# Optimization experiments

Measured on AMD Instinct MI355X. Metric: run time of the kernel, lower is better.

## Reference

```python
import jax, jax.numpy as jnp
import numpy as np
from jax import lax


def _l2n(t, eps=1e-12):
    n = jnp.sqrt(jnp.sum(t * t, axis=-1, keepdims=True))
    return t / jnp.maximum(n, eps)


def _ln(t, w, b, eps=1e-5):
    mu = jnp.mean(t, -1, keepdims=True)
    var = jnp.var(t, -1, keepdims=True)
    return (t - mu) / jnp.sqrt(var + eps) * w + b


def _unfold3(x):
    # nn.Unfold(kernel_size=3, padding=1, stride=1): [B,C,H,W] -> [B,C,9,H*W]
    B, C, H, W = x.shape
    xp = jnp.pad(x, ((0, 0), (0, 0), (1, 1), (1, 1)))
    pat = jnp.stack([xp[:, :, i:i + H, j:j + W] for i in range(3) for j in range(3)], axis=2)
    return pat.reshape(B, C, 9, H * W)


def _forward(x, norm1_w, norm1_b, q_w, q_b, kv_w, kv_b, temperature, query_embedding,
             learnable_tokens, learnable_bias, sr_w, sr_b, pln_w, pln_b, proj_w, proj_b,
             norm2_w, norm2_b, fc1_w, fc1_b, dw_w, dw_b, fc2_w, fc2_b):
    B, C, H, W = x.shape
    nh = temperature.shape[0]
    d = C // nh
    N = H * W
    K = 9  # local_len = window_size**2
    # norm1 (WithBias LayerNorm over channel dim, channels-last)
    y = _ln(x.reshape(B, C, N).transpose(0, 2, 1), norm1_w, norm1_b)  # [B,N,C]
    # ---- AggregatedAttention ----
    q = (y @ q_w.T + q_b).reshape(B, N, nh, d).transpose(0, 2, 1, 3)  # [B,h,N,d]
    qn = _l2n(q)
    qs = (qn + query_embedding) * jax.nn.softplus(temperature)
    kv = y @ kv_w.T + kv_b  # [B,N,2C]
    k_loc = _l2n(kv[..., :C].reshape(B, N, nh, d)).reshape(B, N, C)
    kvl = jnp.concatenate([k_loc, kv[..., C:]], -1).transpose(0, 2, 1).reshape(B, 2 * C, H, W)
    pat = _unfold3(kvl).reshape(B, 2 * nh, d, K, N).transpose(0, 1, 4, 2, 3)  # [B,2h,N,d,K]
    k_l, v_l = pat[:, :nh], pat[:, nh:]
    attn_local = jnp.einsum('bhnd,bhndk->bhnk', qs, k_l)  # [B,h,N,K]
    # pooled branch; sr_ratio=1 so adaptive_avg_pool2d is identity
    y4 = y.transpose(0, 2, 1).reshape(B, C, H, W)
    xp = jax.nn.gelu(jnp.einsum('oc,bchw->bohw', sr_w, y4) + sr_b[:, None, None], approximate=False)
    xp = _ln(xp.reshape(B, C, N).transpose(0, 2, 1), pln_w, pln_b)  # [B,pool_len,C]
    kvp = (xp @ kv_w.T + kv_b).reshape(B, N, 2 * nh, d).transpose(0, 2, 1, 3)
    k_p = _l2n(kvp[:, :nh])
    v_p = kvp[:, nh:]
    attn_pool = jnp.einsum('bhnd,bhmd->bhnm', qs, k_p)  # [B,h,N,pool_len]
    attn = jax.nn.softmax(jnp.concatenate([attn_local, attn_pool], -1), axis=-1)
    a_l, a_p = attn[..., :K], attn[..., K:]
    w_l = jnp.einsum('bhnd,hdk->bhnk', qn, learnable_tokens) + learnable_bias + a_l
    x_local = jnp.einsum('bhnk,bhndk->bhnd', w_l, v_l)
    x_pool = jnp.einsum('bhnm,bhmd->bhnd', a_p, v_p)
    xo = (x_local + x_pool).transpose(0, 2, 1, 3).reshape(B, N, C)
    # proj then raw torch-style reshape [B,N,C] -> [B,C,H,W] (memory reinterpretation)
    xo = (xo @ proj_w.T + proj_b).reshape(B, C, H, W)
    x = x + xo
    # ---- ConvolutionalGLU MLP ----
    hf = dw_b.shape[0]
    y2 = _ln(x.reshape(B, C, N).transpose(0, 2, 1), norm2_w, norm2_b).transpose(0, 2, 1).reshape(B, C, H, W)
    f1 = jnp.einsum('oc,bchw->bohw', fc1_w, y2) + fc1_b[:, None, None]
    a, v = f1[:, :hf], f1[:, hf:]
    dw = lax.conv_general_dilated(a, dw_w, (1, 1), ((1, 1), (1, 1)),
                                  feature_group_count=hf,
                                  dimension_numbers=('NCHW', 'OIHW', 'NCHW')) + dw_b[:, None, None]
    g = jax.nn.gelu(dw, approximate=False) * v
    out = jnp.einsum('oc,bchw->bohw', fc2_w, g) + fc2_b[:, None, None]
    return x + out


def setup_inputs() -> dict:
    key = jax.random.key(0)
    B, C, H, W = 2, 128, 56, 56
    nh, d, K = 4, 32, 9
    hf = int(2 * int(C * 4.0) / 3)  # 341
    ks = iter(jax.random.split(key, 16))
    rn = lambda shape, s=0.02: jax.random.normal(next(ks), shape, jnp.float32) * s
    return {
        'x': jax.random.normal(next(ks), (B, C, H, W), jnp.float32),
        'norm1_w': jnp.ones((C,), jnp.float32), 'norm1_b': jnp.zeros((C,), jnp.float32),
        'q_w': rn((C, C)), 'q_b': jnp.zeros((C,), jnp.float32),
        'kv_w': rn((2 * C, C)), 'kv_b': jnp.zeros((2 * C,), jnp.float32),
        'temperature': jnp.full((nh, 1, 1), float(np.log(np.exp(1.0 / 0.24) - 1.0)), jnp.float32),
        'query_embedding': rn((nh, 1, d)),
        'learnable_tokens': rn((nh, d, K)),
        'learnable_bias': jnp.zeros((nh, 1, K), jnp.float32),
        'sr_w': rn((C, C)), 'sr_b': jnp.zeros((C,), jnp.float32),
        'pln_w': jnp.ones((C,), jnp.float32), 'pln_b': jnp.zeros((C,), jnp.float32),
        'proj_w': rn((C, C)), 'proj_b': jnp.zeros((C,), jnp.float32),
        'norm2_w': jnp.ones((C,), jnp.float32), 'norm2_b': jnp.zeros((C,), jnp.float32),
        'fc1_w': rn((2 * hf, C)), 'fc1_b': jnp.zeros((2 * hf,), jnp.float32),
        'dw_w': rn((hf, 1, 3, 3)), 'dw_b': jnp.zeros((hf,), jnp.float32),
        'fc2_w': rn((C, hf)), 'fc2_b': jnp.zeros((C,), jnp.float32),
    }


def reference(x, norm1_w, norm1_b, q_w, q_b, kv_w, kv_b, temperature, query_embedding,
              learnable_tokens, learnable_bias, sr_w, sr_b, pln_w, pln_b, proj_w, proj_b,
              norm2_w, norm2_b, fc1_w, fc1_b, dw_w, dw_b, fc2_w, fc2_b):
    return _forward(x, norm1_w, norm1_b, q_w, q_b, kv_w, kv_b, temperature, query_embedding,
                    learnable_tokens, learnable_bias, sr_w, sr_b, pln_w, pln_b, proj_w, proj_b,
                    norm2_w, norm2_b, fc1_w, fc1_b, dw_w, dw_b, fc2_w, fc2_b)
```

## Files before the change

kernel.cpp:

```cpp
#include <hip/hip_runtime.h>
#include <hip/hip_bf16.h>

typedef __hip_bfloat16 bf16;
typedef short s8v __attribute__((ext_vector_type(8)));
typedef short s4v __attribute__((ext_vector_type(4)));
typedef float f4v __attribute__((ext_vector_type(4)));

#define DEVI __device__ __forceinline__

DEVI float cvt(float x){ return x; }
DEVI float cvt(bf16 x){ return __bfloat162float(x); }

DEVI void stg(float* p, float v){ *p = v; }
DEVI void stg(bf16* p, float v){ *p = __float2bfloat16(v); }

DEVI float gelu_exact(float x){
  return 0.5f*x*(1.0f + erff(x*0.70710678118654752440f));
}

constexpr int B_ = 2, C_ = 128, H_ = 56, W_ = 56, N_ = 3136, NH_ = 4, D_ = 32, HF_ = 341;
constexpr int ROWS_ = B_*N_;
constexpr int KF2 = 352;
constexpr int GQ_ = NH_*B_*N_;
constexpr int FW = 512;
constexpr int KSP = 8;
constexpr int SPLIT = 384;
constexpr int NTILE = 392;
constexpr float LOG2E = 1.4426950408889634f;
constexpr float E8L2  = 11.541560327111707f;

DEVI void ln_tile_body(int tile, int t, const float* __restrict__ x,
                       const float* __restrict__ w, const float* __restrict__ bia,
                       bf16* __restrict__ y, float* sm , float* st )
{
  int b = tile / 196, nb = (tile % 196) * 16;
  {
    int c = t >> 1, half = t & 1;
    const float* xp = x + ((long)b*C_ + c)*N_ + nb + half*8;
    f4v v0 = *(const f4v*)xp;
    f4v v1 = *(const f4v*)(xp + 4);
    #pragma unroll
    for (int j=0;j<4;j++){
      sm[c*17 + half*8 + j    ] = v0[j];
      sm[c*17 + half*8 + 4 + j] = v1[j];
    }
  }
  __syncthreads();
  {
    int i = t >> 4, k = t & 15;
    float s = 0.f, ss = 0.f;
    #pragma unroll
    for (int u=0;u<8;u++){
      float v = sm[(k + u*16)*17 + i];
      s += v; ss = fmaf(v,v,ss);
    }
    #pragma unroll
    for (int off=1; off<16; off<<=1){
      s  += __shfl_xor(s,  off);
      ss += __shfl_xor(ss, off);
    }
    if (k == 0){
      float mu  = s*(1.0f/128.0f);
      float var = fmaxf(ss*(1.0f/128.0f) - mu*mu, 0.f);
      st[i]      = mu;
      st[16 + i] = rsqrtf(var + 1e-5f);
    }
  }
  __syncthreads();
  {
    int i = t >> 4, c0 = (t & 15)*8;
    float mu = st[i], inv = st[16 + i];
    bf16 o8[8];
    #pragma unroll
    for (int j=0;j<8;j++){
      int c = c0 + j;
      o8[j] = __float2bfloat16((sm[c*17 + i] - mu)*inv*w[c] + bia[c]);
    }
    *(s8v*)(y + ((long)(b*N_ + nb + i))*C_ + c0) = *(const s8v*)o8;
  }
}

__global__ __launch_bounds__(256)
void ln_tile_kernel(const float* __restrict__ x, const float* __restrict__ w,
                    const float* __restrict__ bia, bf16* __restrict__ y)
{
  __shared__ float sm[128*17];
  __shared__ float st[32];
  ln_tile_body(blockIdx.x, threadIdx.x, x, w, bia, y, sm, st);
}

__global__ __launch_bounds__(256)
void head_kernel(const float* __restrict__ q_w, const float* __restrict__ kv_w,
                 const float* __restrict__ sr_w, const float* __restrict__ proj_w,
                 const float* __restrict__ fc1_w, const float* __restrict__ fc2_w,
                 const float* __restrict__ q_b, const float* __restrict__ kv_b,
                 const float* __restrict__ sr_b, const float* __restrict__ tokens,
                 bf16* __restrict__ out, float* __restrict__ bias_out,
                 float* __restrict__ tokt,
                 const float* __restrict__ x_in, const float* __restrict__ n1w,
                 const float* __restrict__ n1b, bf16* __restrict__ y)
{
  __shared__ float sm[128*17];
  __shared__ float st[32];
  if (blockIdx.x >= 216){
    ln_tile_body(blockIdx.x - 216, threadIdx.x, x_in, n1w, n1b, y, sm, st);
    return;
  }
  int t = blockIdx.x*256 + threadIdx.x;
  if (t < 42304){
    int t0 = t*4;
    const float* src;
    if      (t0 <  16384) src = q_w    + t0;
    else if (t0 <  49152) src = kv_w   + (t0-16384);
    else if (t0 <  65536) src = sr_w   + (t0-49152);
    else if (t0 <  81920) src = proj_w + (t0-65536);
    else                  src = fc1_w  + (t0-81920);
    f4v v = *(const f4v*)src;
    bf16 o4[4];
    #pragma unroll
    for (int j=0;j<4;j++) o4[j] = __float2bfloat16(v[j]);
    *(s4v*)(out + t0) = *(const s4v*)o4;
  } else if (t < 53568){
    int i = (t - 42304)*4;
    int m = i / KF2, kp = i % KF2;
    bf16 o4[4];
    #pragma unroll
    for (int j=0;j<4;j++)
      o4[j] = __float2bfloat16((kp+j < HF_) ? fc2_w[m*HF_ + kp + j] : 0.f);
    *(s4v*)(out + 169216 + i) = *(const s4v*)o4;
  } else if (t < 54080){
    int i = t - 53568;
    float bv = (i < 128) ? q_b[i] : (i < 384) ? kv_b[i-128] : sr_b[i-384];
    bias_out[i] = bv;
  } else if (t < 55232){
    int i = t - 54080;
    int hk = i >> 5, d = i & 31;
    int h = hk / 9, k = hk - h*9;
    tokt[i] = tokens[(h*D_ + d)*9 + k];
  }
}

template<int KT, int MODE, typename TC, int BM=64, int LDA=KT, int NCH=1>
__global__ __launch_bounds__(256)
void gemm_mfma(const bf16* __restrict__ A, const bf16* __restrict__ B,
               const float* __restrict__ bias, const float* __restrict__ res,
               TC* __restrict__ Cm, int M, int Nn,
               long sA, long sB, long sC, long sR,
               const float* __restrict__ qe, const float* __restrict__ temp,
               bf16* __restrict__ aux0, bf16* __restrict__ aux1)
{
  A  += (long)blockIdx.z * sA;
  B  += (long)blockIdx.z * sB;
  Cm += (long)blockIdx.z * sC;
  if (res) res += (long)blockIdx.z * sR;
  int lane = threadIdx.x & 63, w = threadIdx.x >> 6;
  int m = lane & 15, quad = lane >> 4;
  int n0 = blockIdx.x*64, m0 = blockIdx.y*BM;
  const bf16* ap[NCH];
  #pragma unroll
  for (int cc=0; cc<NCH; cc++){
    int ar = m0 + cc*64 + w*16 + m;
    if (ar >= M) ar = M-1;
    ap[cc] = A + (long)ar*LDA + quad*8;
  }
  const bf16* bp = B + (long)(n0 + m)*KT + quad*8;
  s8v a4[KT/32];
  if (MODE==7){
    float s=0.f, ssum=0.f;
    #pragma unroll
    for (int i=0;i<KT/32;i++){
      a4[i] = *(const s8v*)(ap[0] + i*32);
      #pragma unroll
      for (int j=0;j<8;j++){
        float v = cvt(((const bf16*)&a4[i])[j]);
        s += v; ssum = fmaf(v,v,ssum);
      }
    }
    s    += __shfl_xor(s,16);    s    += __shfl_xor(s,32);
    ssum += __shfl_xor(ssum,16); ssum += __shfl_xor(ssum,32);
    float mu  = s*(1.0f/128.0f);
    float var = fmaxf(ssum*(1.0f/128.0f) - mu*mu, 0.f);
    float inv = rsqrtf(var + 1e-5f);
    #pragma unroll
    for (int i=0;i<KT/32;i++){
      #pragma unroll
      for (int j=0;j<8;j++){
        int c = i*32 + quad*8 + j;
        float v = cvt(((const bf16*)&a4[i])[j]);
        ((bf16*)&a4[i])[j] = __float2bfloat16((v-mu)*inv*qe[c] + temp[c]);
      }
    }
  }
  f4v acc[NCH][4];
  #pragma unroll
  for (int cc=0; cc<NCH; cc++)
    #pragma unroll
    for (int s=0;s<4;s++) acc[cc][s] = (f4v){0.f,0.f,0.f,0.f};
  __builtin_amdgcn_s_setprio(1);
  #pragma unroll
  for (int k0 = 0; k0 < KT; k0 += 32){
    s8v bf[4];
    #pragma unroll
    for (int s=0;s<4;s++) bf[s] = *(const s8v*)(bp + (long)s*16*KT + k0);
    #pragma unroll
    for (int cc=0; cc<NCH; cc++){
      s8v af = (MODE==7) ? a4[k0/32] : *(const s8v*)(ap[cc] + k0);
      #pragma unroll
      for (int s=0;s<4;s++)
        acc[cc][s] = __builtin_amdgcn_mfma_f32_16x16x32_bf16(af, bf[s], acc[cc][s], 0, 0, 0);
    }
  }
  __builtin_amdgcn_s_setprio(0);
  if ((MODE==6 || MODE==7) && blockIdx.x < 2){
    int hA = blockIdx.x*2, hB = hA+1;
    float spA = 0.f, spB = 0.f;
    if (MODE==6){
      spA = log1pf(expf(temp[hA])) * LOG2E;
      spB = log1pf(expf(temp[hB])) * LOG2E;
    }
    #pragma unroll
    for (int cc=0; cc<NCH; cc++){
      #pragma unroll
      for (int r=0;r<4;r++){
        float v4[4];
        #pragma unroll
        for (int s=0;s<4;s++) v4[s] = acc[cc][s][r] + bias[n0 + s*16 + m];
        float ssA = v4[0]*v4[0] + v4[1]*v4[1];
        float ssB = v4[2]*v4[2] + v4[3]*v4[3];
        #pragma unroll
        for (int off=1; off<16; off<<=1){
          ssA += __shfl_xor(ssA, off);
          ssB += __shfl_xor(ssB, off);
        }
        float invA = 1.f/fmaxf(sqrtf(ssA), 1e-12f);
        float invB = 1.f/fmaxf(sqrtf(ssB), 1e-12f);
        int gm = m0 + cc*64 + w*16 + quad*4 + r;
        int b = gm / N_, n = gm % N_;
        #pragma unroll
        for (int s=0;s<4;s++){
          int h = (s<2) ? hA : hB;
          int d = (s&1)*16 + m;
          float v = v4[s] * ((s<2) ? invA : invB);
          if (MODE==6) v = (v + qe[h*D_ + d]) * ((s<2) ? spA : spB);
          aux0[((long)(b*NH_+h)*N_ + n)*D_ + d] = __float2bfloat16(v);
        }
      }
    }
    return;
  }
  if (MODE==6 && blockIdx.x >= 2 && blockIdx.x < 4){
    #pragma unroll
    for (int cc=0; cc<NCH; cc++){
      #pragma unroll
      for (int r=0;r<4;r++){
        float v4[4];
        #pragma unroll
        for (int s=0;s<4;s++) v4[s] = acc[cc][s][r] + bias[n0 + s*16 + m];
        float ssA = v4[0]*v4[0] + v4[1]*v4[1];
        float ssB = v4[2]*v4[2] + v4[3]*v4[3];
        #pragma unroll
        for (int off=1; off<16; off<<=1){
          ssA += __shfl_xor(ssA, off);
          ssB += __shfl_xor(ssB, off);
        }
        float invA = 1.f/fmaxf(sqrtf(ssA), 1e-12f);
        float invB = 1.f/fmaxf(sqrtf(ssB), 1e-12f);
        int gm = m0 + cc*64 + w*16 + quad*4 + r;
        #pragma unroll
        for (int s=0;s<4;s++){
          float v = v4[s] * ((s<2) ? invA : invB);
          stg(&Cm[(long)gm*Nn + n0 + s*16 + m], v);
        }
      }
    }
    return;
  }
  if (MODE==7){
    int gm0 = m0 + w*16 + quad*4;
    int b = gm0 / N_, nb = gm0 % N_;
    #pragma unroll
    for (int s=0;s<4;s++){
      int h = (blockIdx.x-2)*2 + (s>>1);
      int d = (s&1)*16 + m;
      bf16 p4[4];
      #pragma unroll
      for (int r=0;r<4;r++) p4[r] = __float2bfloat16(acc[0][s][r] + bias[n0 + s*16 + m]);
      *(s4v*)(aux1 + ((long)(b*NH_+h)*D_ + d)*N_ + nb) = *(const s4v*)p4;
    }
    return;
  }
  #pragma unroll
  for (int cc=0; cc<NCH; cc++){
    int m0c = m0 + cc*64;
    #pragma unroll
    for (int s=0;s<4;s++){
      int gn = n0 + s*16 + m;
      #pragma unroll
      for (int r=0;r<4;r++){
        int gm = m0c + w*16 + quad*4 + r;
        if (gm >= M) continue;
        float v = acc[cc][s][r];
        if (MODE==1 || MODE==4 || MODE==6) v += bias[gn];
        else                               v += bias[gm];
        if (MODE==6 && gn >= 384) v = gelu_exact(v);
        if (MODE==4 || MODE==5) v += res[(long)gm*Nn + gn];
        stg(&Cm[(long)gm*Nn + gn], v);
      }
    }
  }
}

__global__ __launch_bounds__(256)
void attn_part_kernel(const bf16* __restrict__ qs_, const bf16* __restrict__ kp_,
                      const bf16* __restrict__ vp_,
                      bf16* __restrict__ Op, float* __restrict__ Lp)
{
  int bh = blockIdx.y;
  int z  = blockIdx.z;
  int lane = threadIdx.x & 63;
  int w    = threadIdx.x >> 6;
  int m    = lane & 15, quad = lane >> 4;
  int base = blockIdx.x*256 + w*16;

  s8v af[4]; bool hasQ[4];
  #pragma unroll
  for (int ch=0; ch<4; ch++){
    int qq = base + ch*64;
    hasQ[ch] = (qq < N_);
    af[ch] = *(const s8v*)(qs_ + ((long)bh*N_ + (hasQ[ch] ? qq : base) + m)*D_ + quad*8);
  }
  const bf16* kpb = kp_ + (long)bh*N_*D_;
  const bf16* vpb = vp_ + (long)bh*D_*N_;
  int kperm = (m & 3) + 8*(m >> 2);
  const f4v CINIT = {-E8L2, -E8L2, -E8L2, -E8L2};
  f4v o0[4], o1[4];
  float l[4];
  #pragma unroll
  for (int ch=0; ch<4; ch++){
    o0[ch] = (f4v){0.f,0.f,0.f,0.f}; o1[ch] = (f4v){0.f,0.f,0.f,0.f};
    l[ch] = 0.f;
  }

  auto loadKV = [&](s8v* kf, s8v* vf, int t){
    kf[0] = *(const s8v*)(kpb + (long)(t + kperm     )*D_ + quad*8);
    kf[1] = *(const s8v*)(kpb + (long)(t + kperm +  4)*D_ + quad*8);
    kf[2] = *(const s8v*)(kpb + (long)(t + kperm + 32)*D_ + quad*8);
    kf[3] = *(const s8v*)(kpb + (long)(t + kperm + 36)*D_ + quad*8);
    vf[0] = *(const s8v*)(vpb + (long)(m     )*N_ + t      + quad*8);
    vf[1] = *(const s8v*)(vpb + (long)(16 + m)*N_ + t      + quad*8);
    vf[2] = *(const s8v*)(vpb + (long)(m     )*N_ + t + 32 + quad*8);
    vf[3] = *(const s8v*)(vpb + (long)(16 + m)*N_ + t + 32 + quad*8);
  };
  auto compute = [&](const s8v* kf, const s8v* vf){
    __builtin_amdgcn_s_setprio(1);
    #pragma unroll
    for (int ch=0; ch<4; ch++){
      f4v c[4];
      #pragma unroll
      for (int s=0;s<4;s++)
        c[s] = __builtin_amdgcn_mfma_f32_16x16x32_bf16(kf[s], af[ch], CINIT, 0, 0, 0);
      bf16 p8a[8], p8b[8];
      float ls = 0.f;
      #pragma unroll
      for (int r=0;r<4;r++){
        float ea = __builtin_amdgcn_exp2f(c[0][r]);
        float eb = __builtin_amdgcn_exp2f(c[1][r]);
        float ec = __builtin_amdgcn_exp2f(c[2][r]);
        float ed = __builtin_amdgcn_exp2f(c[3][r]);
        ls += (ea+eb) + (ec+ed);
        p8a[r] = __float2bfloat16(ea); p8a[4+r] = __float2bfloat16(eb);
        p8b[r] = __float2bfloat16(ec); p8b[4+r] = __float2bfloat16(ed);
      }
      l[ch] += ls;
      s8v pa = *(const s8v*)p8a, pb = *(const s8v*)p8b;
      o0[ch] = __builtin_amdgcn_mfma_f32_16x16x32_bf16(pa, vf[0], o0[ch], 0, 0, 0);
      o1[ch] = __builtin_amdgcn_mfma_f32_16x16x32_bf16(pa, vf[1], o1[ch], 0, 0, 0);
      o0[ch] = __builtin_amdgcn_mfma_f32_16x16x32_bf16(pb, vf[2], o0[ch], 0, 0, 0);
      o1[ch] = __builtin_amdgcn_mfma_f32_16x16x32_bf16(pb, vf[3], o1[ch], 0, 0, 0);
    }
    __builtin_amdgcn_s_setprio(0);
  };

  int tlo = z*SPLIT, thi = (z==KSP-1) ? N_ : tlo + SPLIT;
  s8v kfA[4], vfA[4], kfB[4], vfB[4];
  int t0 = tlo;
  loadKV(kfA, vfA, t0);
  for (;;){
    if (t0 + 64 < thi) loadKV(kfB, vfB, t0 + 64);
    compute(kfA, vfA);
    t0 += 64;
    if (t0 >= thi) break;
    if (t0 + 64 < thi) loadKV(kfA, vfA, t0 + 64);
    compute(kfB, vfB);
    t0 += 64;
    if (t0 >= thi) break;
  }
  #pragma unroll
  for (int ch=0; ch<4; ch++){
    if (!hasQ[ch]) continue;
    float lr = l[ch];
    lr += __shfl_xor(lr, 16);
    lr += __shfl_xor(lr, 32);
    long gqBase = (long)bh*N_ + base + ch*64;
    #pragma unroll
    for (int r=0;r<4;r++){
      bf16* op = Op + ((long)z*GQ_ + gqBase + quad*4 + r)*32;
      op[m]      = __float2bfloat16(o0[ch][r]);
      op[16 + m] = __float2bfloat16(o1[ch][r]);
    }
    if (quad == 0) Lp[(long)z*GQ_ + gqBase + m] = lr;
  }
}

__global__ __launch_bounds__(256)
void attn_combine_kernel(const bf16* __restrict__ Op, const float* __restrict__ Lp,
                         const bf16* __restrict__ qs_, const bf16* __restrict__ fused,
                         const float* __restrict__ qe, const float* __restrict__ temp,
                         const float* __restrict__ tokt, const float* __restrict__ tbias,
                         bf16* __restrict__ xo)
{
  int t  = blockIdx.x*256 + threadIdx.x;
  int gq = t >> 3;
  int l8 = t & 7;
  int d0 = l8*4;
  int n = gq % N_; int bh = gq / N_; int h = bh & 3; int b = bh >> 2;
  float out[4] = {0.f,0.f,0.f,0.f};
  #pragma unroll
  for (int z=0; z<KSP; z++){
    s4v o4 = *(const s4v*)(Op + ((long)z*GQ_ + gq)*32 + d0);
    #pragma unroll
    for (int j=0;j<4;j++) out[j] += cvt(((const bf16*)&o4)[j]);
  }
  float L = Lp[(long)l8*GQ_ + gq];
  #pragma unroll
  for (int off=1; off<8; off<<=1) L += __shfl_xor(L, off);
  float q[4];
  {
    s4v q4 = *(const s4v*)(qs_ + (long)gq*D_ + d0);
    #pragma unroll
    for (int j=0;j<4;j++) q[j] = cvt(((const bf16*)&q4)[j]) * 0.6931471805599453f;
  }
  int hy = n / W_, wx = n % W_;
  const bf16* kvb = fused + (long)b*N_*FW + 128 + h*D_ + d0;
  float el[9];
  #pragma unroll
  for (int k=0;k<9;k++){
    int di = k/3-1, dj = k%3-1;
    int yy = hy+di, xx = wx+dj;
    bool ok = (yy>=0 && yy<H_ && xx>=0 && xx<W_);
    float dot = 0.f;
    if (ok){
      s4v k4 = *(const s4v*)(kvb + (long)(yy*W_+xx)*FW);
      #pragma unroll
      for (int j=0;j<4;j++)
        dot = fmaf(q[j], cvt(((const bf16*)&k4)[j]), dot);
    }
    #pragma unroll
    for (int off=1; off<8; off<<=1) dot += __shfl_xor(dot, off);
    el[k] = __expf(dot - 8.f);
    L += el[k];
  }
  float invL = 1.f/L;
  #pragma unroll
  for (int j=0;j<4;j++) out[j] *= invL;
  float sp = log1pf(expf(temp[h]));
  float invsp = 1.f/sp;
  float qn[4];
  #pragma unroll
  for (int j=0;j<4;j++) qn[j] = q[j]*invsp - qe[h*D_ + d0 + j];
  const float* tk = tokt + (long)h*9*D_ + d0;
  #pragma unroll
  for (int k=0;k<9;k++){
    f4v tv = *(const f4v*)(tk + k*D_);
    float tok = qn[0]*tv[0] + qn[1]*tv[1] + qn[2]*tv[2] + qn[3]*tv[3];
    #pragma unroll
    for (int off=1; off<8; off<<=1) tok += __shfl_xor(tok, off);
    float wl = tok + tbias[h*9+k] + el[k]*invL;
    int di = k/3-1, dj = k%3-1;
    int yy = hy+di, xx = wx+dj;
    if (yy>=0 && yy<H_ && xx>=0 && xx<W_){
      s4v v4 = *(const s4v*)(kvb + (long)(yy*W_+xx)*FW + 128);
      #pragma unroll
      for (int j=0;j<4;j++) out[j] = fmaf(wl, cvt(((const bf16*)&v4)[j]), out[j]);
    }
  }
  bf16 o4[4];
  #pragma unroll
  for (int j=0;j<4;j++) o4[j] = __float2bfloat16(out[j]);
  *(s4v*)(xo + ((long)(b*N_ + n))*C_ + h*D_ + d0) = *(const s4v*)o4;
}

__global__ __launch_bounds__(256)
void dwconv_kernel(const bf16* __restrict__ f1, const float* __restrict__ dww,
                   const float* __restrict__ dwb, bf16* __restrict__ g)
{
  __shared__ bf16 sg[32*72];
  int bx = blockIdx.x;
  int ntile = bx % 49;
  int cg    = (bx / 49) % 11;
  int b     = bx / (49*11);
  int t = threadIdx.x;
  f1 += (long)b*2*HF_*N_;
  {
    int c_local = t & 31, chun = t >> 5;
    int c = cg*32 + c_local;
    int n0 = ntile*64 + chun*8;
    int y = n0 / W_, x0 = n0 % W_;
    bf16 o8[8];
    if (c < HF_){
      const bf16* ap = f1 + (long)c*N_;
      float acc[8];
      #pragma unroll
      for (int j=0;j<8;j++) acc[j] = dwb[c];
      #pragma unroll
      for (int dy=-1; dy<=1; dy++){
        int yy = y + dy;
        if (yy < 0 || yy >= H_) continue;
        int base = yy*W_ + x0;
        s8v mid = *(const s8v*)(ap + base);
        float wnd[10];
        wnd[0] = (x0 > 0)      ? cvt(ap[base-1]) : 0.f;
        #pragma unroll
        for (int j=0;j<8;j++) wnd[1+j] = cvt(((const bf16*)&mid)[j]);
        wnd[9] = (x0 + 8 < W_) ? cvt(ap[base+8]) : 0.f;
        float k0 = dww[c*9 + (dy+1)*3    ];
        float k1 = dww[c*9 + (dy+1)*3 + 1];
        float k2 = dww[c*9 + (dy+1)*3 + 2];
        #pragma unroll
        for (int j=0;j<8;j++)
          acc[j] = fmaf(k0, wnd[j], fmaf(k1, wnd[j+1], fmaf(k2, wnd[j+2], acc[j])));
      }
      s8v g8 = *(const s8v*)(f1 + (long)(HF_+c)*N_ + n0);
      #pragma unroll
      for (int j=0;j<8;j++)
        o8[j] = __float2bfloat16(gelu_exact(acc[j]) * cvt(((const bf16*)&g8)[j]));
    } else {
      #pragma unroll
      for (int j=0;j<8;j++) o8[j] = __float2bfloat16(0.f);
    }
    *(s8v*)(&sg[c_local*72 + chun*8]) = *(const s8v*)o8;
  }
  __syncthreads();
  {
    int n_local = t >> 2, c0 = (t & 3)*8;
    bf16 o8[8];
    #pragma unroll
    for (int j=0;j<8;j++) o8[j] = sg[(c0+j)*72 + n_local];
    *(s8v*)(g + (long)b*N_*KF2 + (long)(ntile*64 + n_local)*KF2 + cg*32 + c0)
        = *(const s8v*)o8;
  }
}

extern "C" void kernel_launch(void* const* d_in, const int* in_sizes, int n_in,
                              void* d_out, int out_size, void* d_ws, size_t ws_size,
                              hipStream_t stream)
{
  (void)in_sizes; (void)n_in; (void)out_size; (void)ws_size;
  const float* x_in      = (const float*)d_in[0];
  const float* norm1_w   = (const float*)d_in[1];
  const float* norm1_b   = (const float*)d_in[2];
  const float* q_w       = (const float*)d_in[3];
  const float* q_b       = (const float*)d_in[4];
  const float* kv_w      = (const float*)d_in[5];
  const float* kv_b      = (const float*)d_in[6];
  const float* temp      = (const float*)d_in[7];
  const float* qe        = (const float*)d_in[8];
  const float* tokens    = (const float*)d_in[9];
  const float* tbias     = (const float*)d_in[10];
  const float* sr_w      = (const float*)d_in[11];
  const float* sr_b      = (const float*)d_in[12];
  const float* pln_w     = (const float*)d_in[13];
  const float* pln_b     = (const float*)d_in[14];
  const float* proj_w    = (const float*)d_in[15];
  const float* proj_b    = (const float*)d_in[16];
  const float* norm2_w   = (const float*)d_in[17];
  const float* norm2_b   = (const float*)d_in[18];
  const float* fc1_w     = (const float*)d_in[19];
  const float* fc1_b     = (const float*)d_in[20];
  const float* dw_w      = (const float*)d_in[21];
  const float* dw_b      = (const float*)d_in[22];
  const float* fc2_w     = (const float*)d_in[23];
  const float* fc2_b     = (const float*)d_in[24];

  char* w8 = (char*)d_ws;
  bf16*  fused   = (bf16*)(w8 + 0);
  float* x2      = (float*)(w8 + 0);
  bf16*  y2      = (bf16*)(w8 + 3211264);
  bf16*  f1b     = (bf16*)(w8 + 4816896);
  bf16*  qs      = (bf16*)(w8 + 6422528);
  bf16*  k_p     = (bf16*)(w8 + 9633792);
  bf16*  v_p     = (bf16*)(w8 + 11239424);
  bf16*  Opart   = (bf16*)(w8 + 13045056);
  bf16*  g_rows  = (bf16*)(w8 + 32312640);
  bf16*  wbase   = (bf16*)(w8 + 36728128);
  float* fbias   = (float*)(w8 + 37156672);
  float* tokt    = (float*)(w8 + 37158720);
  bf16*  y       = f1b;
  bf16*  xo      = (bf16*)d_out;
  float* Lpart   = (float*)((char*)d_out + 1605632);
  bf16*  proj_wb = wbase + 65536;
  bf16*  fc1_wb  = wbase + 81920;
  bf16*  fc2_wb  = wbase + 169216;

  head_kernel<<<216 + NTILE, 256, 0, stream>>>(
      q_w, kv_w, sr_w, proj_w, fc1_w, fc2_w, q_b, kv_b, sr_b, tokens,
      wbase, fbias, tokt, x_in, norm1_w, norm1_b, y);
  gemm_mfma<128, 6, bf16, 128, 128, 2><<<dim3(8,49), 256, 0, stream>>>(
      y, wbase, fbias, nullptr, fused, ROWS_, FW, 0,0,0,0, qe, temp, qs, nullptr);
  gemm_mfma<128, 7, bf16, 64, FW><<<dim3(4,98), 256, 0, stream>>>(
      fused + 384, wbase + 16384, kv_b, nullptr, (bf16*)nullptr, ROWS_, 256, 0,0,0,0,
      pln_w, pln_b, k_p, v_p);
  attn_part_kernel<<<dim3(13,8,KSP), 256, 0, stream>>>(qs, k_p, v_p, Opart, Lpart);
  attn_combine_kernel<<<GQ_*8/256, 256, 0, stream>>>(Opart, Lpart, qs, fused,
                                                     qe, temp, tokt, tbias, xo);
  gemm_mfma<128, 4, float, 16><<<dim3(2,392), 64, 0, stream>>>(
      xo, proj_wb, proj_b, x_in, x2, ROWS_, 128, 0,0,0,0, nullptr, nullptr, nullptr, nullptr);
  ln_tile_kernel<<<NTILE, 256, 0, stream>>>(x2, norm2_w, norm2_b, y2);
  gemm_mfma<128, 3, bf16, 128, 128, 2><<<dim3(49,6,B_), 256, 0, stream>>>(
      fc1_wb, y2, fc1_b, nullptr, f1b, 2*HF_, N_,
      0, (long)N_*C_, (long)2*HF_*N_, 0, nullptr, nullptr, nullptr, nullptr);
  dwconv_kernel<<<B_*11*49, 256, 0, stream>>>(f1b, dw_w, dw_b, g_rows);
  gemm_mfma<KF2, 5, float, 16><<<dim3(49,8,B_), 64, 0, stream>>>(
      fc2_wb, g_rows, fc2_b, x2, (float*)d_out, C_, N_,
      0, (long)N_*KF2, (long)C_*N_, (long)C_*N_, nullptr, nullptr, nullptr, nullptr);
}
```

Measured before the change: 219.1 us.

## Fuse pooled-KV GEMM, attention, combine and proj into persistent mega-kernel with grid barriers

```diff
diff --git a/kernel.cpp b/kernel.cpp
--- a/kernel.cpp
+++ b/kernel.cpp
@@ -26,8 +26,24 @@
 constexpr int KSP = 8;
 constexpr int SPLIT = 384;
 constexpr int NTILE = 392;
+constexpr int MEGA_NB = 832;
 constexpr float LOG2E = 1.4426950408889634f;
 constexpr float E8L2  = 11.541560327111707f;
+
+DEVI void grid_barrier(unsigned* bar, unsigned target, int t){
+  __syncthreads();
+  if (t == 0){
+    __hip_atomic_fetch_add(bar, 1u, __ATOMIC_RELEASE, __HIP_MEMORY_SCOPE_AGENT);
+    long it = 0;
+    for (;;){
+      unsigned v = __hip_atomic_load(bar, __ATOMIC_ACQUIRE, __HIP_MEMORY_SCOPE_AGENT);
+      if (v >= target) break;
+      __builtin_amdgcn_s_sleep(2);
+      if (++it >= 1000000L) break;
+    }
+  }
+  __syncthreads();
+}
 
 DEVI void ln_tile_body(int tile, int t, const float* __restrict__ x,
                        const float* __restrict__ w, const float* __restrict__ bia,
@@ -96,7 +112,7 @@
                  const float* __restrict__ q_b, const float* __restrict__ kv_b,
                  const float* __restrict__ sr_b, const float* __restrict__ tokens,
                  bf16* __restrict__ out, float* __restrict__ bias_out,
-                 float* __restrict__ tokt,
+                 float* __restrict__ tokt, unsigned* __restrict__ barc,
                  const float* __restrict__ x_in, const float* __restrict__ n1w,
                  const float* __restrict__ n1b, bf16* __restrict__ y)
 {
@@ -137,6 +153,8 @@
     int hk = i >> 5, d = i & 31;
     int h = hk / 9, k = hk - h*9;
     tokt[i] = tokens[(h*D_ + d)*9 + k];
+  } else if (t < 55236){
+    barc[t - 55232] = 0u;
   }
 }
 
@@ -164,33 +182,6 @@
     ap[cc] = A + (long)ar*LDA + quad*8;
   }
   const bf16* bp = B + (long)(n0 + m)*KT + quad*8;
-  s8v a4[KT/32];
-  if (MODE==7){
-    float s=0.f, ssum=0.f;
-    #pragma unroll
-    for (int i=0;i<KT/32;i++){
-      a4[i] = *(const s8v*)(ap[0] + i*32);
-      #pragma unroll
-      for (int j=0;j<8;j++){
-        float v = cvt(((const bf16*)&a4[i])[j]);
-        s += v; ssum = fmaf(v,v,ssum);
-      }
-    }
-    s    += __shfl_xor(s,16);    s    += __shfl_xor(s,32);
-    ssum += __shfl_xor(ssum,16); ssum += __shfl_xor(ssum,32);
-    float mu  = s*(1.0f/128.0f);
-    float var = fmaxf(ssum*(1.0f/128.0f) - mu*mu, 0.f);
-    float inv = rsqrtf(var + 1e-5f);
-    #pragma unroll
-    for (int i=0;i<KT/32;i++){
-      #pragma unroll
-      for (int j=0;j<8;j++){
-        int c = i*32 + quad*8 + j;
-        float v = cvt(((const bf16*)&a4[i])[j]);
-        ((bf16*)&a4[i])[j] = __float2bfloat16((v-mu)*inv*qe[c] + temp[c]);
-      }
-    }
-  }
   f4v acc[NCH][4];
   #pragma unroll
   for (int cc=0; cc<NCH; cc++)
@@ -204,20 +195,17 @@
     for (int s=0;s<4;s++) bf[s] = *(const s8v*)(bp + (long)s*16*KT + k0);
     #pragma unroll
     for (int cc=0; cc<NCH; cc++){
-      s8v af = (MODE==7) ? a4[k0/32] : *(const s8v*)(ap[cc] + k0);
+      s8v af = *(const s8v*)(ap[cc] + k0);
       #pragma unroll
       for (int s=0;s<4;s++)
         acc[cc][s] = __builtin_amdgcn_mfma_f32_16x16x32_bf16(af, bf[s], acc[cc][s], 0, 0, 0);
     }
   }
   __builtin_amdgcn_s_setprio(0);
-  if ((MODE==6 || MODE==7) && blockIdx.x < 2){
+  if (MODE==6 && blockIdx.x < 2){
     int hA = blockIdx.x*2, hB = hA+1;
-    float spA = 0.f, spB = 0.f;
-    if (MODE==6){
-      spA = log1pf(expf(temp[hA])) * LOG2E;
-      spB = log1pf(expf(temp[hB])) * LOG2E;
-    }
+    float spA = log1pf(expf(temp[hA])) * LOG2E;
+    float spB = log1pf(expf(temp[hB])) * LOG2E;
     #pragma unroll
     for (int cc=0; cc<NCH; cc++){
       #pragma unroll
@@ -241,7 +229,7 @@
           int h = (s<2) ? hA : hB;
           int d = (s&1)*16 + m;
           float v = v4[s] * ((s<2) ? invA : invB);
-          if (MODE==6) v = (v + qe[h*D_ + d]) * ((s<2) ? spA : spB);
+          v = (v + qe[h*D_ + d]) * ((s<2) ? spA : spB);
           aux0[((long)(b*NH_+h)*N_ + n)*D_ + d] = __float2bfloat16(v);
         }
       }
@@ -275,20 +263,6 @@
     }
     return;
   }
-  if (MODE==7){
-    int gm0 = m0 + w*16 + quad*4;
-    int b = gm0 / N_, nb = gm0 % N_;
-    #pragma unroll
-    for (int s=0;s<4;s++){
-      int h = (blockIdx.x-2)*2 + (s>>1);
-      int d = (s&1)*16 + m;
-      bf16 p4[4];
-      #pragma unroll
-      for (int r=0;r<4;r++) p4[r] = __float2bfloat16(acc[0][s][r] + bias[n0 + s*16 + m]);
-      *(s4v*)(aux1 + ((long)(b*NH_+h)*D_ + d)*N_ + nb) = *(const s4v*)p4;
-    }
-    return;
-  }
   #pragma unroll
   for (int cc=0; cc<NCH; cc++){
     int m0c = m0 + cc*64;
@@ -310,17 +284,107 @@
   }
 }
 
-__global__ __launch_bounds__(256)
-void attn_part_kernel(const bf16* __restrict__ qs_, const bf16* __restrict__ kp_,
-                      const bf16* __restrict__ vp_,
-                      bf16* __restrict__ Op, float* __restrict__ Lp)
-{
-  int bh = blockIdx.y;
-  int z  = blockIdx.z;
-  int lane = threadIdx.x & 63;
-  int w    = threadIdx.x >> 6;
+
+DEVI void gemm7_body(int bx, int by, int t,
+                     const bf16* A , const bf16* __restrict__ Bw,
+                     const float* __restrict__ bias,
+                     const float* __restrict__ pw, const float* __restrict__ pb,
+                     bf16* __restrict__ k_p, bf16* __restrict__ v_p)
+{
+  int lane = t & 63, w = t >> 6;
+  int m = lane & 15, quad = lane >> 4;
+  int n0 = bx*64, m0 = by*64;
+  int ar = m0 + w*16 + m;
+  const bf16* ap = A + (long)ar*FW + quad*8;
+  const bf16* bp = Bw + (long)(n0 + m)*128 + quad*8;
+  s8v a4[4];
+  float s=0.f, ssum=0.f;
+  #pragma unroll
+  for (int i=0;i<4;i++){
+    a4[i] = *(const s8v*)(ap + i*32);
+    #pragma unroll
+    for (int j=0;j<8;j++){
+      float v = cvt(((const bf16*)&a4[i])[j]);
+      s += v; ssum = fmaf(v,v,ssum);
+    }
+  }
+  s    += __shfl_xor(s,16);    s    += __shfl_xor(s,32);
+  ssum += __shfl_xor(ssum,16); ssum += __shfl_xor(ssum,32);
+  float mu  = s*(1.0f/128.0f);
+  float var = fmaxf(ssum*(1.0f/128.0f) - mu*mu, 0.f);
+  float inv = rsqrtf(var + 1e-5f);
+  #pragma unroll
+  for (int i=0;i<4;i++)
+    #pragma unroll
+    for (int j=0;j<8;j++){
+      int c = i*32 + quad*8 + j;
+      float v = cvt(((const bf16*)&a4[i])[j]);
+      ((bf16*)&a4[i])[j] = __float2bfloat16((v-mu)*inv*pw[c] + pb[c]);
+    }
+  f4v acc[4];
+  #pragma unroll
+  for (int si=0;si<4;si++) acc[si] = (f4v){0.f,0.f,0.f,0.f};
+  __builtin_amdgcn_s_setprio(1);
+  #pragma unroll
+  for (int k0=0;k0<128;k0+=32){
+    s8v af = a4[k0/32];
+    #pragma unroll
+    for (int si=0;si<4;si++){
+      s8v bf = *(const s8v*)(bp + (long)si*16*128 + k0);
+      acc[si] = __builtin_amdgcn_mfma_f32_16x16x32_bf16(af, bf, acc[si], 0, 0, 0);
+    }
+  }
+  __builtin_amdgcn_s_setprio(0);
+  if (bx < 2){
+    int hA = bx*2, hB = hA+1;
+    #pragma unroll
+    for (int r=0;r<4;r++){
+      float v4[4];
+      #pragma unroll
+      for (int si=0;si<4;si++) v4[si] = acc[si][r] + bias[n0 + si*16 + m];
+      float ssA = v4[0]*v4[0] + v4[1]*v4[1];
+      float ssB = v4[2]*v4[2] + v4[3]*v4[3];
+      #pragma unroll
+      for (int off=1; off<16; off<<=1){
+        ssA += __shfl_xor(ssA, off);
+        ssB += __shfl_xor(ssB, off);
+      }
+      float invA = 1.f/fmaxf(sqrtf(ssA), 1e-12f);
+      float invB = 1.f/fmaxf(sqrtf(ssB), 1e-12f);
+      int gm = m0 + w*16 + quad*4 + r;
+      int b = gm / N_, n = gm % N_;
+      #pragma unroll
+      for (int si=0;si<4;si++){
+        int h = (si<2) ? hA : hB;
+        int d = (si&1)*16 + m;
+        float v = v4[si] * ((si<2) ? invA : invB);
+        k_p[((long)(b*NH_+h)*N_ + n)*D_ + d] = __float2bfloat16(v);
+      }
+    }
+  } else {
+    int gm0 = m0 + w*16 + quad*4;
+    int b = gm0 / N_, nb = gm0 % N_;
+    #pragma unroll
+    for (int si=0;si<4;si++){
+      int h = (bx-2)*2 + (si>>1);
+      int d = (si&1)*16 + m;
+      bf16 p4[4];
+      #pragma unroll
+      for (int r=0;r<4;r++) p4[r] = __float2bfloat16(acc[si][r] + bias[n0 + si*16 + m]);
+      *(s4v*)(v_p + ((long)(b*NH_+h)*D_ + d)*N_ + nb) = *(const s4v*)p4;
+    }
+  }
+}
+
+DEVI void attn_part_body(int bx, int bh, int z, int tid,
+                         const bf16* __restrict__ qs_, const bf16* __restrict__ kp_,
+                         const bf16* __restrict__ vp_,
+                         bf16* __restrict__ Op, float* __restrict__ Lp)
+{
+  int lane = tid & 63;
+  int w    = tid >> 6;
   int m    = lane & 15, quad = lane >> 4;
-  int base = blockIdx.x*256 + w*16;
+  int base = bx*256 + w*16;
 
   s8v af[4]; bool hasQ[4];
   #pragma unroll
@@ -412,14 +476,14 @@
   }
 }
 
-__global__ __launch_bounds__(256)
-void attn_combine_kernel(const bf16* __restrict__ Op, const float* __restrict__ Lp,
-                         const bf16* __restrict__ qs_, const bf16* __restrict__ fused,
-                         const float* __restrict__ qe, const float* __restrict__ temp,
-                         const float* __restrict__ tokt, const float* __restrict__ tbias,
-                         bf16* __restrict__ xo)
-{
-  int t  = blockIdx.x*256 + threadIdx.x;
+DEVI void combine_body(int vb, int tid,
+                       const bf16* __restrict__ Op, const float* __restrict__ Lp,
+                       const bf16* __restrict__ qs_, const bf16* fused,
+                       const float* __restrict__ qe, const float* __restrict__ temp,
+                       const float* __restrict__ tokt, const float* __restrict__ tbias,
+                       bf16* __restrict__ xo)
+{
+  int t  = vb*256 + tid;
   int gq = t >> 3;
   int l8 = t & 7;
   int d0 = l8*4;
@@ -488,6 +552,71 @@
   #pragma unroll
   for (int j=0;j<4;j++) o4[j] = __float2bfloat16(out[j]);
   *(s4v*)(xo + ((long)(b*N_ + n))*C_ + h*D_ + d0) = *(const s4v*)o4;
+}
+
+DEVI void proj_body(int bx, int by, int tid,
+                    const bf16* __restrict__ A , const bf16* __restrict__ Bw,
+                    const float* __restrict__ bias, const float* __restrict__ res,
+                    float* x2)
+{
+  int m = tid & 15, quad = tid >> 4;
+  int n0 = bx*64, m0 = by*16;
+  const bf16* ap = A + (long)(m0 + m)*128 + quad*8;
+  const bf16* bp = Bw + (long)(n0 + m)*128 + quad*8;
+  f4v acc[4];
+  #pragma unroll
+  for (int s=0;s<4;s++) acc[s] = (f4v){0.f,0.f,0.f,0.f};
+  __builtin_amdgcn_s_setprio(1);
+  #pragma unroll
+  for (int k0=0;k0<128;k0+=32){
+    s8v af = *(const s8v*)(ap + k0);
+    #pragma unroll
+    for (int s=0;s<4;s++){
+      s8v bf = *(const s8v*)(bp + (long)s*16*128 + k0);
+      acc[s] = __builtin_amdgcn_mfma_f32_16x16x32_bf16(af, bf, acc[s], 0, 0, 0);
+    }
+  }
+  __builtin_amdgcn_s_setprio(0);
+  #pragma unroll
+  for (int s=0;s<4;s++){
+    int gn = n0 + s*16 + m;
+    #pragma unroll
+    for (int r=0;r<4;r++){
+      int gm = m0 + quad*4 + r;
+      x2[(long)gm*128 + gn] = acc[s][r] + bias[gn] + res[(long)gm*128 + gn];
+    }
+  }
+}
+
+__global__ __launch_bounds__(256, 4)
+void attn_mega_kernel(const bf16* fused, const bf16* __restrict__ kv_wb,
+                      const float* __restrict__ kv_b,
+                      const float* __restrict__ pln_w, const float* __restrict__ pln_b,
+                      bf16* __restrict__ k_p, bf16* __restrict__ v_p,
+                      const bf16* __restrict__ qs, bf16* __restrict__ Op,
+                      float* __restrict__ Lp,
+                      const float* __restrict__ qe, const float* __restrict__ temp,
+                      const float* __restrict__ tokt, const float* __restrict__ tbias,
+                      bf16* __restrict__ xo,
+                      const bf16* __restrict__ proj_wb, const float* __restrict__ proj_b,
+                      const float* __restrict__ x_in, float* x2,
+                      unsigned* barc)
+{
+  int rb = blockIdx.x, t = threadIdx.x;
+  if (rb < 392) gemm7_body(rb & 3, rb >> 2, t, fused + 384, kv_wb, kv_b,
+                           pln_w, pln_b, k_p, v_p);
+  grid_barrier(barc, 1*MEGA_NB, t);
+  {
+    int bx = rb % 13; int rem = rb / 13;
+    attn_part_body(bx, rem & 7, rem >> 3, t, qs, k_p, v_p, Op, Lp);
+  }
+  grid_barrier(barc, 2*MEGA_NB, t);
+  if (rb < 784) combine_body(rb, t, Op, Lp, qs, fused, qe, temp, tokt, tbias, xo);
+  grid_barrier(barc, 3*MEGA_NB, t);
+  if (rb < 196){
+    int vb = rb*4 + (t >> 6);
+    proj_body(vb & 1, vb >> 1, t & 63, xo, proj_wb, proj_b, x_in, x2);
+  }
 }
 
 __global__ __launch_bounds__(256)
@@ -595,6 +724,7 @@
   bf16*  wbase   = (bf16*)(w8 + 36728128);
   float* fbias   = (float*)(w8 + 37156672);
   float* tokt    = (float*)(w8 + 37158720);
+  unsigned* barc = (unsigned*)(w8 + 37163328);
   bf16*  y       = f1b;
   bf16*  xo      = (bf16*)d_out;
   float* Lpart   = (float*)((char*)d_out + 1605632);
@@ -604,17 +734,12 @@
 
   head_kernel<<<216 + NTILE, 256, 0, stream>>>(
       q_w, kv_w, sr_w, proj_w, fc1_w, fc2_w, q_b, kv_b, sr_b, tokens,
-      wbase, fbias, tokt, x_in, norm1_w, norm1_b, y);
+      wbase, fbias, tokt, barc, x_in, norm1_w, norm1_b, y);
   gemm_mfma<128, 6, bf16, 128, 128, 2><<<dim3(8,49), 256, 0, stream>>>(
       y, wbase, fbias, nullptr, fused, ROWS_, FW, 0,0,0,0, qe, temp, qs, nullptr);
-  gemm_mfma<128, 7, bf16, 64, FW><<<dim3(4,98), 256, 0, stream>>>(
-      fused + 384, wbase + 16384, kv_b, nullptr, (bf16*)nullptr, ROWS_, 256, 0,0,0,0,
-      pln_w, pln_b, k_p, v_p);
-  attn_part_kernel<<<dim3(13,8,KSP), 256, 0, stream>>>(qs, k_p, v_p, Opart, Lpart);
-  attn_combine_kernel<<<GQ_*8/256, 256, 0, stream>>>(Opart, Lpart, qs, fused,
-                                                     qe, temp, tokt, tbias, xo);
-  gemm_mfma<128, 4, float, 16><<<dim3(2,392), 64, 0, stream>>>(
-      xo, proj_wb, proj_b, x_in, x2, ROWS_, 128, 0,0,0,0, nullptr, nullptr, nullptr, nullptr);
+  attn_mega_kernel<<<MEGA_NB, 256, 0, stream>>>(
+      fused, wbase + 16384, kv_b, pln_w, pln_b, k_p, v_p, qs, Opart, Lpart,
+      qe, temp, tokt, tbias, xo, proj_wb, proj_b, x_in, x2, barc);
   ln_tile_kernel<<<NTILE, 256, 0, stream>>>(x2, norm2_w, norm2_b, y2);
   gemm_mfma<128, 3, bf16, 128, 128, 2><<<dim3(49,6,B_), 256, 0, stream>>>(
       fc1_wb, y2, fc1_b, nullptr, f1b, 2*HF_, N_,
```

New measurement: 800.6 us. +265.3%, slower.
